# Kernel optimization log

Hardware: AMD Instinct MI355X
Metric: run time of the kernel (lower is better)

Reference implementation:

```python
import jax, jax.numpy as jnp
import numpy as np
import math

# Static config derived from init_kwargs
B, L, D, H, NL = 256, 256, 128, 2, 2
E = D // H                       # 64
F = L // 2 + 1                   # 129 rfft bins
SR = 0.6                         # sample_ratio (> 1/n_layers)
STEP = (F * (1.0 - SR)) // (NL - 1)          # 51.0, python float floor-div as in torch code
LEFTS = [int(F * (1.0 - SR) - k * STEP) for k in range(NL)]   # [51, 0]
RIGHTS = [int(F - k * STEP) for k in range(NL)]               # [129, 78]
TOPK = max(int(1 * math.log(L)), 1)          # factor=1 -> 5
NUM_TOTAL = 100000                           # user_num + item_num
SPATIAL_RATIO = 0.1
INV_SQRT_E = 1.0 / math.sqrt(E)
INV_SQRT_2 = 1.0 / math.sqrt(2.0)


def setup_inputs() -> dict:
    key = jax.random.key(0)
    ks = jax.random.split(key, 12)
    s = 0.05
    return {
        "paths": jax.random.randint(ks[0], (B, L), 0, NUM_TOTAL),
        "lengths": jax.random.randint(ks[1], (B,), 1, L + 1),
        "degrees": jax.random.randint(ks[2], (B,), 0, 64),
        "training": 1,
        "ego_emb": jax.random.normal(ks[3], (NUM_TOTAL + 1, D), jnp.float32) * s,
        "pos_emb": jax.random.normal(ks[4], (L, D), jnp.float32) * s,
        "Wq": jax.random.normal(ks[5], (NL, D, D), jnp.float32) * s,
        "Wk": jax.random.normal(ks[6], (NL, D, D), jnp.float32) * s,
        "Wv": jax.random.normal(ks[7], (NL, D, D), jnp.float32) * s,
        "Wp": jax.random.normal(ks[8], (NL, D, D), jnp.float32) * s,
        "F1": jax.random.normal(ks[9], (NL, D, 2 * D), jnp.float32) * s,
        "F2": jax.random.normal(ks[10], (NL, 2 * D, D), jnp.float32) * s,
    }


def _hybrid_attention(k, x, mask, Wq, Wk, Wv, Wp):
    # project and split heads: [B,H,E,L]
    def proj(W):
        return (x @ W).reshape(B, L, H, E).transpose(0, 2, 3, 1)
    q, kk, v = proj(Wq), proj(Wk), proj(Wv)
    qf = jnp.fft.rfft(q, axis=-1)   # [B,H,E,F] complex
    kf = jnp.fft.rfft(kk, axis=-1)
    vf = jnp.fft.rfft(v, axis=-1)
    l, r = LEFTS[k], RIGHTS[k]
    # frequency-band attention: band-limited cross-correlation (scatter back == zero-pad)
    res = qf[..., l:r] * jnp.conj(kf[..., l:r])
    box = jnp.zeros(qf.shape, dtype=res.dtype).at[..., l:r].set(res)
    corr = jnp.fft.irfft(box, n=L, axis=-1)          # [B,H,E,L]
    mean_value = jnp.mean(corr, axis=(1, 2))         # [B,L]
    # training branch: global topk delays (shared across batch), roll-based aggregation
    _, delays = jax.lax.top_k(jnp.mean(mean_value, axis=0), TOPK)   # [TOPK]
    weights = mean_value[:, delays]                  # [B,TOPK]
    tmp_corr = jax.nn.softmax(weights, axis=-1)      # [B,TOPK]
    # roll(v, -d) along time == gather at (t + d) % L
    idx = (jnp.arange(L)[None, :] + delays[:, None]) % L            # [TOPK,L]
    gathered = v[:, :, :, idx]                       # [B,H,E,TOPK,L]
    freq = jnp.einsum('bhetl,bt->bhel', gathered, tmp_corr)
    freq = freq.transpose(0, 3, 1, 2).reshape(B, L, D)
    # dual-domain: time attention on band-limited signals (std=True -> same band)
    def band_ifft(f):
        padded = jnp.zeros(f.shape, dtype=f.dtype).at[..., l:r].set(f[..., l:r])
        return jnp.fft.irfft(padded, n=L, axis=-1).transpose(0, 1, 3, 2)   # [B,H,L,E]
    qt, kt, vt = band_ifft(qf), band_ifft(kf), band_ifft(vf)
    scores = jnp.einsum('bhqe,bhke->bhqk', qt, kt) * INV_SQRT_E + mask
    att = jax.nn.softmax(scores, axis=-1)
    spatial = jnp.einsum('bhqk,bhke->bhqe', att, vt).transpose(0, 2, 1, 3).reshape(B, L, D)
    out = (1.0 - SPATIAL_RATIO) * freq + SPATIAL_RATIO * spatial
    return out @ Wp + x


def reference(paths, lengths, degrees, training, ego_emb, pos_emb, Wq, Wk, Wv, Wp, F1, F2):
    del degrees, training  # degrees unused; training branch baked in (training=True)
    x = ego_emb[paths] + pos_emb[None, :, :]         # [B,L,D]
    m = (paths < NUM_TOTAL).astype(jnp.float32)
    mask = ((1.0 - m) * -10000.0)[:, None, None, :]  # [B,1,1,L]
    for k in range(NL):
        a = _hybrid_attention(k, x, mask, Wq[k], Wk[k], Wv[k], Wp[k])
        h = a @ F1[k]
        h = h * 0.5 * (1.0 + jax.lax.erf(h * INV_SQRT_2))   # exact GELU
        x = h @ F2[k]
    # gather last valid position per sequence
    return x[jnp.arange(B), lengths - 1]             # [B,D]
```

## Files before the change

### kernel.cpp

```cpp
#include <hip/hip_runtime.h>
#include <math.h>

#define Bn 256
#define Ln 256
#define Dn 128
#define Hn 2
#define En 64
#define NLn 2
#define TOPKn 5
#define NUM_TOTALn 100000
#define BLD (Bn*Ln*Dn)
#define WT_LAYER 147456

using frag_ab = __attribute__((ext_vector_type(8))) short;
using frag_cd = __attribute__((ext_vector_type(4))) float;

__device__ inline short f2bf(float f) {
    union { float f; unsigned u; } c; c.f = f;
    unsigned r = (c.u + 0x7FFFu + ((c.u >> 16) & 1u)) >> 16;
    return (short)r;
}
__device__ inline float bf2f(short s) {
    union { unsigned u; float f; } c; c.u = ((unsigned)(unsigned short)s) << 16;
    return c.f;
}

__global__ void beacon_kernel(float* out, float v) { out[0] = v; }

__global__ __launch_bounds__(256) void build_G_kernel(short* __restrict__ G) {
    int k = blockIdx.x, t = blockIdx.y, s = threadIdx.x;
    int d = (t - s) & 255;
    int f1 = (k == 0) ? 51 : 1;
    int f2 = (k == 0) ? 127 : 77;
    float acc;
    if (d == 0) {
        acc = 2.0f * (float)(f2 - f1 + 1);
    } else {
        const float c = 3.14159265358979323846f / 256.0f;
        int ahi = (d * (2 * f2 + 1)) & 511;
        int alo = (d * (2 * f1 - 1)) & 511;
        acc = (sinf(c * (float)ahi) - sinf(c * (float)alo)) / sinf(c * (float)d);
    }
    acc += (k == 0) ? ((d & 1) ? -1.0f : 1.0f)
                    : 1.0f;
    G[((size_t)k * 256 + t) * 256 + s] = f2bf(acc * (1.0f / 256.0f));
}

__global__ __launch_bounds__(256) void build_x_kernel(const int* __restrict__ paths,
                                                      const float* __restrict__ ego,
                                                      const float* __restrict__ pos,
                                                      short* __restrict__ x) {
    int base = (blockIdx.x * 256 + threadIdx.x) * 4;
    int d = base & 127;
    int bl = base >> 7;
    int t = bl & 255;
    float4 e = *(const float4*)(ego + (size_t)paths[bl] * Dn + d);
    float4 p = *(const float4*)(pos + t * Dn + d);
    short4 s;
    s.x = f2bf(e.x + p.x); s.y = f2bf(e.y + p.y);
    s.z = f2bf(e.z + p.z); s.w = f2bf(e.w + p.w);
    *(short4*)&x[base] = s;
}

__global__ __launch_bounds__(256) void wtrans_all_kernel(
        const float* __restrict__ Wq, const float* __restrict__ Wk,
        const float* __restrict__ Wv, const float* __restrict__ Wp,
        const float* __restrict__ F1, const float* __restrict__ F2,
        short* __restrict__ Wt) {
    int z = blockIdx.y;
    int idx = blockIdx.x * 256 + threadIdx.x;
    short* WtL = Wt + (size_t)z * WT_LAYER;
    if (idx < 65536) {
        int which = idx >> 14, local = idx & 16383;
        const float* src = (which == 0) ? Wq : (which == 1) ? Wk
                         : (which == 2) ? Wv : Wp;
        float scale = (which == 3) ? 0.1f : 1.0f;
        int n = local & 127, k = local >> 7;
        WtL[(which << 14) + n * 128 + k] = f2bf(scale * src[(size_t)z * 16384 + local]);
    } else if (idx < 98304) {
        int local = idx - 65536;
        int n = local & 255, k = local >> 8;
        WtL[65536 + n * 128 + k] = f2bf(F1[(size_t)z * 32768 + local]);
    } else {
        int local = idx - 98304;
        int n = local & 127, k = local >> 7;
        WtL[98304 + n * 256 + k] = f2bf(F2[(size_t)z * 32768 + local]);
    }
}

template<bool BT_FAST, bool GELU_EPI>
__global__ __launch_bounds__(256)
void mfma_gemm_kernel(const short* A, const short* Bp, short* C, const short* R,
                      int K, int lda, int ldb, int ldc, int ldr,
                      long long sA, long long sB, long long sC, long long sR,
                      long long sCsplit, float alpha, float beta) {
    int bz = blockIdx.z;
    A += (size_t)bz * sA; C += (size_t)bz * sC;
    if (R) R += (size_t)bz * sR;
    const short* Bt = Bp + (size_t)bz * sB;
    const int m0 = blockIdx.x * 128, n0 = blockIdx.y * 128;
    int n0c = n0;
    if (sCsplit) { C += (size_t)blockIdx.y * sCsplit; n0c = 0; }
    __shared__ short As[128 * 40];
    __shared__ short Bs[128 * 40];
    int tid = threadIdx.x;
    int lane = tid & 63, wave = tid >> 6;
    int wr = (wave >> 1) * 64, wc = (wave & 1) * 64;
    int l15 = lane & 15, qd = lane >> 4;

    frag_cd zero4 = {0.f, 0.f, 0.f, 0.f};
    frag_cd acc[4][4];
    #pragma unroll
    for (int i = 0; i < 4; i++)
        #pragma unroll
        for (int j = 0; j < 4; j++) acc[i][j] = zero4;

    int arow = tid >> 1, acg = (tid & 1) * 16;
    int bnrow = tid >> 1, bcg = (tid & 1) * 16;
    int bkk = tid & 31, bnb = (tid >> 5) * 16;

    int4 pa0, pa1, pb0, pb1;
    {
        const short* ap = A + (size_t)(m0 + arow) * lda + acg;
        pa0 = *(const int4*)ap; pa1 = *(const int4*)(ap + 8);
        if (BT_FAST) {
            const short* bp = Bt + (size_t)(n0 + bnrow) * ldb + bcg;
            pb0 = *(const int4*)bp; pb1 = *(const int4*)(bp + 8);
        } else {
            const short* bp = Bt + (size_t)bkk * ldb + n0 + bnb;
            pb0 = *(const int4*)bp; pb1 = *(const int4*)(bp + 8);
        }
    }

    for (int k0 = 0; k0 < K; k0 += 32) {
        __syncthreads();
        *(int4*)&As[arow * 40 + acg] = pa0;
        *(int4*)&As[arow * 40 + acg + 8] = pa1;
        if (BT_FAST) {
            *(int4*)&Bs[bnrow * 40 + bcg] = pb0;
            *(int4*)&Bs[bnrow * 40 + bcg + 8] = pb1;
        } else {
            short tmp[16];
            *(int4*)&tmp[0] = pb0; *(int4*)&tmp[8] = pb1;
            #pragma unroll
            for (int i = 0; i < 16; i++) Bs[(bnb + i) * 40 + bkk] = tmp[i];
        }
        __syncthreads();
        if (k0 + 32 < K) {
            const short* ap = A + (size_t)(m0 + arow) * lda + k0 + 32 + acg;
            pa0 = *(const int4*)ap; pa1 = *(const int4*)(ap + 8);
            if (BT_FAST) {
                const short* bp = Bt + (size_t)(n0 + bnrow) * ldb + k0 + 32 + bcg;
                pb0 = *(const int4*)bp; pb1 = *(const int4*)(bp + 8);
            } else {
                const short* bp = Bt + (size_t)(k0 + 32 + bkk) * ldb + n0 + bnb;
                pb0 = *(const int4*)bp; pb1 = *(const int4*)(bp + 8);
            }
        }
        frag_ab af[4], bf[4];
        #pragma unroll
        for (int ms = 0; ms < 4; ms++)
            af[ms] = *(frag_ab*)&As[(wr + ms * 16 + l15) * 40 + qd * 8];
        #pragma unroll
        for (int ns = 0; ns < 4; ns++)
            bf[ns] = *(frag_ab*)&Bs[(wc + ns * 16 + l15) * 40 + qd * 8];
        #pragma unroll
        for (int ms = 0; ms < 4; ms++)
            #pragma unroll
            for (int ns = 0; ns < 4; ns++)
                acc[ms][ns] = __builtin_amdgcn_mfma_f32_16x16x32_bf16(
                    bf[ns], af[ms], acc[ms][ns], 0, 0, 0);
    }
    #pragma unroll
    for (int ms = 0; ms < 4; ms++) {
        int m = m0 + wr + ms * 16 + l15;
        #pragma unroll
        for (int ns = 0; ns < 4; ns++) {
            int nb = wc + ns * 16 + qd * 4;
            float v[4];
            #pragma unroll
            for (int r = 0; r < 4; r++) v[r] = alpha * acc[ms][ns][r];
            if (R) {
                short4 r4 = *(const short4*)&R[(size_t)m * ldr + n0 + nb];
                v[0] += beta * bf2f(r4.x); v[1] += beta * bf2f(r4.y);
                v[2] += beta * bf2f(r4.z); v[3] += beta * bf2f(r4.w);
            }
            if (GELU_EPI) {
                #pragma unroll
                for (int r = 0; r < 4; r++)
                    v[r] = v[r] * 0.5f * (1.0f + erff(v[r] * 0.70710678118654752f));
            }
            short4 o;
            o.x = f2bf(v[0]); o.y = f2bf(v[1]); o.z = f2bf(v[2]); o.w = f2bf(v[3]);
            *(short4*)&C[(size_t)m * ldc + n0c + nb] = o;
        }
    }
}

static inline void mgemm(hipStream_t s, const short* A, const short* B, short* C,
                         const short* R, int M, int N, int K,
                         int lda, int ldb, int ldc, int ldr,
                         long long sA, long long sB, long long sC, long long sR,
                         int batch, float alpha, float beta, bool btFast, bool gelu,
                         long long sCsplit = 0) {
    dim3 grid(M / 128, N / 128, batch), block(256);
    if (btFast) {
        if (gelu) mfma_gemm_kernel<true, true ><<<grid, block, 0, s>>>(A, B, C, R, K, lda, ldb, ldc, ldr, sA, sB, sC, sR, sCsplit, alpha, beta);
        else      mfma_gemm_kernel<true, false><<<grid, block, 0, s>>>(A, B, C, R, K, lda, ldb, ldc, ldr, sA, sB, sC, sR, sCsplit, alpha, beta);
    } else {
        if (gelu) mfma_gemm_kernel<false, true ><<<grid, block, 0, s>>>(A, B, C, R, K, lda, ldb, ldc, ldr, sA, sB, sC, sR, sCsplit, alpha, beta);
        else      mfma_gemm_kernel<false, false><<<grid, block, 0, s>>>(A, B, C, R, K, lda, ldb, ldc, ldr, sA, sB, sC, sR, sCsplit, alpha, beta);
    }
}

__global__ __launch_bounds__(512)
void filtproj_kernel(const short* __restrict__ G, const short* __restrict__ x,
                     const short* __restrict__ W, short* __restrict__ q) {
    int b = blockIdx.x;
    __shared__ short As[256 * 40];
    __shared__ short Bs[128 * 40];
    __shared__ short xf[256 * 136];
    int tid = threadIdx.x;
    int lane = tid & 63, wave = tid >> 6;
    int wr = (wave & 3) * 64, wc = (wave >> 2) * 64;
    int l15 = lane & 15, qd = lane >> 4;
    const short* xb = x + ((size_t)b << 15);

    frag_cd zero4 = {0.f, 0.f, 0.f, 0.f};
    frag_cd acc[4][4];
    #pragma unroll
    for (int i = 0; i < 4; i++)
        #pragma unroll
        for (int j = 0; j < 4; j++) acc[i][j] = zero4;

    int arow = tid >> 1, acg = (tid & 1) * 16;
    int bkk = tid & 31, bnb = (tid >> 5) * 16;

    int4 pa0, pa1, pb0, pb1;
    {
        const short* ap = G + (size_t)arow * 256 + acg;
        pa0 = *(const int4*)ap; pa1 = *(const int4*)(ap + 8);
        if (tid < 256) {
            const short* bp = xb + (size_t)bkk * 128 + bnb;
            pb0 = *(const int4*)bp; pb1 = *(const int4*)(bp + 8);
        }
    }
    for (int k0 = 0; k0 < 256; k0 += 32) {
        __syncthreads();
        *(int4*)&As[arow * 40 + acg] = pa0;
        *(int4*)&As[arow * 40 + acg + 8] = pa1;
        if (tid < 256) {
            short tmp[16];
            *(int4*)&tmp[0] = pb0; *(int4*)&tmp[8] = pb1;
            #pragma unroll
            for (int i = 0; i < 16; i++) Bs[(bnb + i) * 40 + bkk] = tmp[i];
        }
        __syncthreads();
        if (k0 + 32 < 256) {
            const short* ap = G + (size_t)arow * 256 + k0 + 32 + acg;
            pa0 = *(const int4*)ap; pa1 = *(const int4*)(ap + 8);
            if (tid < 256) {
                const short* bp = xb + (size_t)(k0 + 32 + bkk) * 128 + bnb;
                pb0 = *(const int4*)bp; pb1 = *(const int4*)(bp + 8);
            }
        }
        frag_ab af[4], bf[4];
        #pragma unroll
        for (int ms = 0; ms < 4; ms++)
            af[ms] = *(frag_ab*)&As[(wr + ms * 16 + l15) * 40 + qd * 8];
        #pragma unroll
        for (int ns = 0; ns < 4; ns++)
            bf[ns] = *(frag_ab*)&Bs[(wc + ns * 16 + l15) * 40 + qd * 8];
        #pragma unroll
        for (int ms = 0; ms < 4; ms++)
            #pragma unroll
            for (int ns = 0; ns < 4; ns++)
                acc[ms][ns] = __builtin_amdgcn_mfma_f32_16x16x32_bf16(
                    bf[ns], af[ms], acc[ms][ns], 0, 0, 0);
    }
    #pragma unroll
    for (int ms = 0; ms < 4; ms++) {
        int m = wr + ms * 16 + l15;
        #pragma unroll
        for (int ns = 0; ns < 4; ns++) {
            int nb = wc + ns * 16 + qd * 4;
            short4 o;
            o.x = f2bf(acc[ms][ns][0]); o.y = f2bf(acc[ms][ns][1]);
            o.z = f2bf(acc[ms][ns][2]); o.w = f2bf(acc[ms][ns][3]);
            *(short4*)&xf[m * 136 + nb] = o;
        }
    }

    int brow = tid >> 2, bcg = (tid & 3) * 8;
    #pragma unroll 1
    for (int y = 0; y < 3; y++) {
        const short* Bt = W + y * 16384;
        #pragma unroll
        for (int i = 0; i < 4; i++)
            #pragma unroll
            for (int j = 0; j < 4; j++) acc[i][j] = zero4;
        int4 pb = *(const int4*)(Bt + (size_t)brow * 128 + bcg);
        for (int k0 = 0; k0 < 128; k0 += 32) {
            __syncthreads();
            *(int4*)&Bs[brow * 40 + bcg] = pb;
            __syncthreads();
            if (k0 + 32 < 128)
                pb = *(const int4*)(Bt + (size_t)brow * 128 + k0 + 32 + bcg);
            frag_ab af[4], bf[4];
            #pragma unroll
            for (int ms = 0; ms < 4; ms++)
                af[ms] = *(frag_ab*)&xf[(wr + ms * 16 + l15) * 136 + k0 + qd * 8];
            #pragma unroll
            for (int ns = 0; ns < 4; ns++)
                bf[ns] = *(frag_ab*)&Bs[(wc + ns * 16 + l15) * 40 + qd * 8];
            #pragma unroll
            for (int ms = 0; ms < 4; ms++)
                #pragma unroll
                for (int ns = 0; ns < 4; ns++)
                    acc[ms][ns] = __builtin_amdgcn_mfma_f32_16x16x32_bf16(
                        bf[ns], af[ms], acc[ms][ns], 0, 0, 0);
        }
        short* Cy = q + (size_t)y * BLD + ((size_t)b << 15);
        #pragma unroll
        for (int ms = 0; ms < 4; ms++) {
            int m = wr + ms * 16 + l15;
            #pragma unroll
            for (int ns = 0; ns < 4; ns++) {
                int nb = wc + ns * 16 + qd * 4;
                short4 o;
                o.x = f2bf(acc[ms][ns][0]); o.y = f2bf(acc[ms][ns][1]);
                o.z = f2bf(acc[ms][ns][2]); o.w = f2bf(acc[ms][ns][3]);
                *(short4*)&Cy[(size_t)m * 128 + nb] = o;
            }
        }
    }
}

template<bool DUAL, bool GELU_EPI, bool MIXA>
__global__ __launch_bounds__(512)
void bgemm_kernel(const short* __restrict__ A1, const short* __restrict__ B1, int K1,
                  const short* __restrict__ A2, const short* __restrict__ B2, int K2,
                  short* C, const short* __restrict__ R, int ldc, int ldr,
                  long long sCsplit,
                  const float* __restrict__ tc, const int* __restrict__ delays) {
    const int m0 = blockIdx.x * 256;
    int n0c;
    if (sCsplit) { C += (size_t)blockIdx.y * sCsplit; n0c = 0; }
    else         { n0c = blockIdx.y * 128; }
    __shared__ short As[256 * 40];
    __shared__ short Bs[128 * 40];
    int tid = threadIdx.x;
    int lane = tid & 63, wave = tid >> 6;
    int wr = (wave & 3) * 64, wc = (wave >> 2) * 64;
    int l15 = lane & 15, qd = lane >> 4;

    float wj[TOPKn]; int dj[TOPKn];
    if (MIXA) {
        #pragma unroll
        for (int j = 0; j < TOPKn; j++) {
            wj[j] = tc[blockIdx.x * TOPKn + j];
            dj[j] = delays[j];
        }
    }

    frag_cd zero4 = {0.f, 0.f, 0.f, 0.f};
    frag_cd acc[4][4];
    #pragma unroll
    for (int i = 0; i < 4; i++)
        #pragma unroll
        for (int j = 0; j < 4; j++) acc[i][j] = zero4;

    int arow = tid >> 1, acg = (tid & 1) * 16;
    int brow = tid >> 2, bcg = (tid & 3) * 8;

    #pragma unroll
    for (int pass = 0; pass < (DUAL ? 2 : 1); pass++) {
        const short* A = pass ? A2 : A1;
        const short* Bb = (pass ? B2 : B1);
        int K = pass ? K2 : K1;
        const bool domix = MIXA && (pass == 0);
        const short* Bt = Bb + (size_t)blockIdx.y * 128 * K;
        const short* xb = A + ((size_t)m0 << 7);
        int4 pa0, pa1, pb0;
        {
            if (!domix) {
                const short* ap = A + (size_t)(m0 + arow) * K + acg;
                pa0 = *(const int4*)ap; pa1 = *(const int4*)(ap + 8);
            }
            pb0 = *(const int4*)(Bt + (size_t)brow * K + bcg);
        }
        for (int k0 = 0; k0 < K; k0 += 32) {
            __syncthreads();
            if (domix) {
                #pragma unroll
                for (int c = 0; c < 2; c++) {
                    int col = k0 + acg + c * 8;
                    float m8[8] = {0.f, 0.f, 0.f, 0.f, 0.f, 0.f, 0.f, 0.f};
                    #pragma unroll
                    for (int j = 0; j < TOPKn; j++) {
                        frag_ab v = *(const frag_ab*)(xb + (((arow + dj[j]) & 255) << 7) + col);
                        #pragma unroll
                        for (int i = 0; i < 8; i++) m8[i] += wj[j] * bf2f(v[i]);
                    }
                    frag_ab o;
                    #pragma unroll
                    for (int i = 0; i < 8; i++) o[i] = f2bf(m8[i]);
                    *(frag_ab*)&As[arow * 40 + acg + c * 8] = o;
                }
            } else {
                *(int4*)&As[arow * 40 + acg] = pa0;
                *(int4*)&As[arow * 40 + acg + 8] = pa1;
            }
            *(int4*)&Bs[brow * 40 + bcg] = pb0;
            __syncthreads();
            if (k0 + 32 < K) {
                if (!domix) {
                    const short* ap = A + (size_t)(m0 + arow) * K + k0 + 32 + acg;
                    pa0 = *(const int4*)ap; pa1 = *(const int4*)(ap + 8);
                }
                pb0 = *(const int4*)(Bt + (size_t)brow * K + k0 + 32 + bcg);
            }
            frag_ab af[4], bf[4];
            #pragma unroll
            for (int ms = 0; ms < 4; ms++)
                af[ms] = *(frag_ab*)&As[(wr + ms * 16 + l15) * 40 + qd * 8];
            #pragma unroll
            for (int ns = 0; ns < 4; ns++)
                bf[ns] = *(frag_ab*)&Bs[(wc + ns * 16 + l15) * 40 + qd * 8];
            #pragma unroll
            for (int ms = 0; ms < 4; ms++)
                #pragma unroll
                for (int ns = 0; ns < 4; ns++)
                    acc[ms][ns] = __builtin_amdgcn_mfma_f32_16x16x32_bf16(
                        bf[ns], af[ms], acc[ms][ns], 0, 0, 0);
        }
    }
    #pragma unroll
    for (int ms = 0; ms < 4; ms++) {
        int m = m0 + wr + ms * 16 + l15;
        #pragma unroll
        for (int ns = 0; ns < 4; ns++) {
            int nb = wc + ns * 16 + qd * 4;
            float v[4];
            #pragma unroll
            for (int r = 0; r < 4; r++) v[r] = acc[ms][ns][r];
            if (R) {
                short4 r4 = *(const short4*)&R[(size_t)m * ldr + n0c + nb];
                v[0] += bf2f(r4.x); v[1] += bf2f(r4.y);
                v[2] += bf2f(r4.z); v[3] += bf2f(r4.w);
            }
            if (GELU_EPI) {
                #pragma unroll
                for (int r = 0; r < 4; r++)
                    v[r] = v[r] * 0.5f * (1.0f + erff(v[r] * 0.70710678118654752f));
            }
            short4 o;
            o.x = f2bf(v[0]); o.y = f2bf(v[1]); o.z = f2bf(v[2]); o.w = f2bf(v[3]);
            *(short4*)&C[(size_t)m * ldc + n0c + nb] = o;
        }
    }
}

__global__ __launch_bounds__(512, 4) void attn_kernel(short* q,
        const short* __restrict__ kb, const short* __restrict__ vf,
        const int* __restrict__ paths, float* __restrict__ mv2) {
    int h = blockIdx.x, b = blockIdx.y;
    __shared__ short SB[256 * 72];
    __shared__ short ks[64 * 72];
    __shared__ short vT[80 * 72];
    __shared__ float masks[256];
    __shared__ float mvpart[512];
    int tid = threadIdx.x;
    int lane = tid & 63, wave = tid >> 6;
    int l15 = lane & 15, qd = lane >> 4;
    if (tid < 256) masks[tid] = (paths[b * 256 + tid] < NUM_TOTALn) ? 0.0f : -10000.0f;
    {
        int e0 = tid * 2;
        #pragma unroll
        for (int i = 0; i < 2; i++) {
            int e = e0 + i;
            int row = 64 + (e >> 6), col = e & 63;
            vT[row * 72 + col] = (row == 64) ? (short)0x3F80 : (short)0;
        }
    }
    short* qg = q + ((size_t)b << 15) + (size_t)h * 64;
    const short* kg = kb + ((size_t)b << 15) + (size_t)h * 64;
    const short* vg = vf + ((size_t)b << 15) + (size_t)h * 64;

    #pragma unroll
    for (int p = 0; p < 4; p++) {
        int chunk = p * 512 + tid;
        int r = chunk >> 3, cb = (chunk & 7) * 8;
        *(frag_ab*)&SB[r * 72 + cb] = *(const frag_ab*)(qg + (size_t)r * 128 + cb);
    }
    __syncthreads();
    int myrow = wave * 32;
    frag_ab aq[2][2];
    #pragma unroll
    for (int mt = 0; mt < 2; mt++)
        #pragma unroll
        for (int hf = 0; hf < 2; hf++)
            aq[mt][hf] = *(frag_ab*)&SB[(myrow + mt * 16 + l15) * 72 + hf * 32 + qd * 8];

    frag_cd zero4 = {0.f, 0.f, 0.f, 0.f};
    frag_cd oacc[2][5];
    #pragma unroll
    for (int mt = 0; mt < 2; mt++)
        #pragma unroll
        for (int et = 0; et < 5; et++) oacc[mt][et] = zero4;
    float macc = 0.0f;
    int tau = tid & 255, half = tid >> 8;

    for (int jt = 0; jt < 4; jt++) {
        __syncthreads();
        {
            int r = tid >> 3, cb = (tid & 7) * 8;
            *(frag_ab*)&ks[r * 72 + cb] =
                *(const frag_ab*)(kg + (size_t)(jt * 64 + r) * 128 + cb);
            frag_ab v8 = *(const frag_ab*)(vg + (size_t)(jt * 64 + r) * 128 + cb);
            int swz = (((r >> 3) ^ (cb >> 3)) << 3) + (r & 7);
            #pragma unroll
            for (int i = 0; i < 8; i++) vT[(cb + i) * 72 + swz] = v8[i];
        }
        __syncthreads();
        #pragma unroll
        for (int mt = 0; mt < 2; mt++) {
            #pragma unroll
            for (int nt = 0; nt < 4; nt++) {
                frag_ab b0 = *(frag_ab*)&ks[(nt * 16 + l15) * 72 + qd * 8];
                frag_ab b1 = *(frag_ab*)&ks[(nt * 16 + l15) * 72 + 32 + qd * 8];
                frag_cd c = zero4;
                c = __builtin_amdgcn_mfma_f32_16x16x32_bf16(aq[mt][0], b0, c, 0, 0, 0);
                c = __builtin_amdgcn_mfma_f32_16x16x32_bf16(aq[mt][1], b1, c, 0, 0, 0);
                int keyLocal = nt * 16 + l15;
                #pragma unroll
                for (int r = 0; r < 4; r++) {
                    int row = myrow + mt * 16 + qd * 4 + r;
                    int tt = (row - jt * 64 - keyLocal) & 255;
                    SB[tt * 66 + keyLocal] = f2bf(c[r] * 0.125f);
                }
            }
        }
        __syncthreads();
        {
            const int* SD32 = (const int*)&SB[tau * 66 + half * 32];
            #pragma unroll
            for (int i = 0; i < 16; i++) {
                int pk = SD32[i];
                macc += bf2f((short)(pk & 0xFFFF)) + bf2f((short)(pk >> 16));
            }
        }
        #pragma unroll
        for (int mt = 0; mt < 2; mt++) {
            int row = myrow + mt * 16 + l15;
            #pragma unroll
            for (int hf = 0; hf < 2; hf++) {
                int kl0 = hf * 32 + qd * 8;
                frag_ab pfrag;
                #pragma unroll
                for (int j = 0; j < 8; j++) {
                    int kl = kl0 + j;
                    int tt = (row - jt * 64 - kl) & 255;
                    float s = bf2f(SB[tt * 66 + kl]);
                    pfrag[j] = f2bf(__expf(s + masks[jt * 64 + kl]));
                }
                #pragma unroll
                for (int et = 0; et < 5; et++) {
                    int e = et * 16 + l15;
                    int blk = (hf * 4 + qd) ^ ((e >> 3) & 7);
                    frag_ab bv = *(frag_ab*)&vT[e * 72 + (blk << 3)];
                    oacc[mt][et] = __builtin_amdgcn_mfma_f32_16x16x32_bf16(pfrag, bv, oacc[mt][et], 0, 0, 0);
                }
            }
        }
    }
    __syncthreads();
    mvpart[tid] = macc;
    __syncthreads();
    if (tid < 256)
        mv2[(size_t)h * 65536 + b * 256 + tid] =
            (mvpart[tid] + mvpart[tid + 256]) * 0.0625f;
    #pragma unroll
    for (int mt = 0; mt < 2; mt++) {
        #pragma unroll
        for (int r = 0; r < 4; r++) {
            float l = oacc[mt][4][r];
            l = __shfl(l, (lane & 48));
            float inv = 1.0f / l;
            int row = myrow + mt * 16 + qd * 4 + r;
            #pragma unroll
            for (int et = 0; et < 4; et++)
                qg[(size_t)row * 128 + et * 16 + l15] = f2bf(oacc[mt][et][r] * inv);
        }
    }
}

__global__ __launch_bounds__(256) void gm_reduce_kernel(const float* __restrict__ mv2,
                                                        float* __restrict__ gm) {
    int tau = blockIdx.x;
    int b = threadIdx.x;
    __shared__ float red[256];
    red[b] = mv2[b * 256 + tau] + mv2[65536 + b * 256 + tau];
    __syncthreads();
    for (int s = 128; s > 0; s >>= 1) { if (b < s) red[b] += red[b + s]; __syncthreads(); }
    if (b == 0) gm[tau] = red[0] * (1.0f / 256.0f);
}

__global__ __launch_bounds__(256) void topk_softmax_kernel(const float* __restrict__ gm,
                                                           const float* __restrict__ mv2,
                                                           int* __restrict__ delays,
                                                           float* __restrict__ tc) {
    __shared__ float vsh[4];
    __shared__ int ish[4];
    __shared__ int dsh[TOPKn];
    int tid = threadIdx.x;
    int lane = tid & 63, wave = tid >> 6;
    float v = gm[tid];
    for (int t = 0; t < TOPKn; t++) {
        float mv_ = v; int mi = tid;
        #pragma unroll
        for (int s = 32; s > 0; s >>= 1) {
            float v2 = __shfl_xor(mv_, s); int i2 = __shfl_xor(mi, s);
            if (v2 > mv_ || (v2 == mv_ && i2 < mi)) { mv_ = v2; mi = i2; }
        }
        if (lane == 0) { vsh[wave] = mv_; ish[wave] = mi; }
        __syncthreads();
        if (tid == 0) {
            float bv = vsh[0]; int bi = ish[0];
            #pragma unroll
            for (int w = 1; w < 4; w++)
                if (vsh[w] > bv || (vsh[w] == bv && ish[w] < bi)) { bv = vsh[w]; bi = ish[w]; }
            dsh[t] = bi; delays[t] = bi;
        }
        __syncthreads();
        if (tid == dsh[t]) v = -1e30f;
    }
    __syncthreads();
    int b = tid;
    float w[TOPKn];
    float m = -1e30f;
    #pragma unroll
    for (int j = 0; j < TOPKn; j++) {
        w[j] = mv2[b * 256 + dsh[j]] + mv2[65536 + b * 256 + dsh[j]];
        m = fmaxf(m, w[j]);
    }
    float ssum = 0.0f;
    #pragma unroll
    for (int j = 0; j < TOPKn; j++) { w[j] = expf(w[j] - m); ssum += w[j]; }
    #pragma unroll
    for (int j = 0; j < TOPKn; j++) tc[b * TOPKn + j] = w[j] / ssum;
}

__global__ __launch_bounds__(256) void gather_out_kernel(const short* __restrict__ x,
                                                         const int* __restrict__ lengths,
                                                         float* __restrict__ out) {
    int idx = blockIdx.x * 256 + threadIdx.x;
    int d = idx & 127;
    int b = idx >> 7;
    out[idx] = bf2f(x[((size_t)b << 15) + (size_t)(lengths[b] - 1) * Dn + d]);
}

extern "C" void kernel_launch(void* const* d_in, const int* in_sizes, int n_in,
                              void* d_out, int out_size, void* d_ws, size_t ws_size,
                              hipStream_t stream) {
    const int* paths    = (const int*)d_in[0];
    const int* lengths  = (const int*)d_in[1];
    const float* ego    = (const float*)d_in[4];
    const float* pos    = (const float*)d_in[5];
    const float* Wq     = (const float*)d_in[6];
    const float* Wk     = (const float*)d_in[7];
    const float* Wv     = (const float*)d_in[8];
    const float* Wp     = (const float*)d_in[9];
    const float* F1     = (const float*)d_in[10];
    const float* F2     = (const float*)d_in[11];
    float* out = (float*)d_out;

    const size_t need = (size_t)5 * BLD * 2 + 131072 * 2 + 131072 * 4
                        + 256 * 4 + 1280 * 4 + 16 * 4 + (size_t)NLn * WT_LAYER * 2;
    if (ws_size < need) {
        beacon_kernel<<<dim3(1), dim3(1), 0, stream>>>(out, (float)(ws_size >> 20));
        return;
    }

    short* x    = (short*)d_ws;
    short* q    = x + (size_t)1 * BLD;
    short* kb   = x + (size_t)2 * BLD;
    short* vf   = x + (size_t)3 * BLD;
    short* x5   = x + (size_t)4 * BLD;
    short* Gb   = x + (size_t)5 * BLD;
    float* mv   = (float*)(Gb + 131072);
    float* gm   = mv + 131072;
    float* tc   = gm + 256;
    int* delays = (int*)(tc + 1280);
    short* Wt   = (short*)(delays + 16);

    build_G_kernel<<<dim3(2, 256), dim3(256), 0, stream>>>(Gb);
    build_x_kernel<<<dim3(BLD / 1024), dim3(256), 0, stream>>>(paths, ego, pos, x);

    wtrans_all_kernel<<<dim3(512, NLn), dim3(256), 0, stream>>>(Wq, Wk, Wv, Wp, F1, F2, Wt);
    mgemm(stream, Wt + 49152, Wt + 32768, Wt + 131072, nullptr,
          128, 128, 128, 128, 128, 128, 0,
          WT_LAYER, WT_LAYER, WT_LAYER, 0, NLn,
          9.0f, 0.0f, false, false);

    for (int k = 0; k < NLn; k++) {
        const short* WtL = Wt + (size_t)k * WT_LAYER;
        filtproj_kernel<<<dim3(256), dim3(512), 0, stream>>>(
            Gb + (size_t)k * 65536, x, WtL, q);

        attn_kernel<<<dim3(2, 256), dim3(512), 0, stream>>>(q, kb, vf, paths, mv);

        gm_reduce_kernel<<<dim3(256), dim3(256), 0, stream>>>(mv, gm);
        topk_softmax_kernel<<<dim3(1), dim3(256), 0, stream>>>(gm, mv, delays, tc);

        bgemm_kernel<true, false, true><<<dim3(256, 1), dim3(512), 0, stream>>>(
            x, WtL + 131072, 128, q, WtL + 49152, 128, kb, x, 128, 128, 0,
            tc, delays);
        bgemm_kernel<false, true, false><<<dim3(256, 2), dim3(512), 0, stream>>>(
            kb, WtL + 65536, 128, nullptr, nullptr, 0, vf, nullptr, 256, 0, 0,
            nullptr, nullptr);
        bgemm_kernel<false, false, false><<<dim3(256, 1), dim3(512), 0, stream>>>(
            vf, WtL + 98304, 256, nullptr, nullptr, 0, x, nullptr, 128, 0, 0,
            nullptr, nullptr);
    }

    gather_out_kernel<<<dim3((Bn * Dn) / 256), dim3(256), 0, stream>>>(x, lengths, out);
}
```

Baseline: 378.4 us.

## Fuse FFN up-projection, GELU and down-projection into one kernel

Replaces the two FFN GEMM launches (F1 with GELU epilogue, then F2) with a single kernel per 256-row tile. The GELU-activated hidden activations stay in shared memory in two 128-column halves, which avoids writing and rereading the 256-wide intermediate through global memory and saves one launch per layer. In exchange the block uses about 140KB of shared memory, which limits occupancy to one block per CU, and the FFN now runs on 256 blocks instead of 512+256.

```diff
diff --git a/kernel.cpp b/kernel.cpp
--- a/kernel.cpp
+++ b/kernel.cpp
@@ -336,6 +336,124 @@
     }
 }
 
+__global__ __launch_bounds__(512)
+void ffn_kernel(const short* __restrict__ a, const short* __restrict__ W,
+                short* __restrict__ x) {
+    int b = blockIdx.x;
+    __shared__ short aL[256 * 132];
+    __shared__ short hA[256 * 132];
+    __shared__ short Bs[128 * 36];
+    int tid = threadIdx.x;
+    int lane = tid & 63, wave = tid >> 6;
+    int wr = (wave & 3) * 64, wc = (wave >> 2) * 64;
+    int l15 = lane & 15, qd = lane >> 4;
+    const short* ab = a + ((size_t)b << 15);
+    const short* F1T = W + 65536;
+    const short* F2T = W + 98304;
+
+    #pragma unroll
+    for (int p = 0; p < 8; p++) {
+        int chunk = p * 512 + tid;
+        int r = chunk >> 4, cb = (chunk & 15) * 8;
+        *(frag_ab*)&aL[r * 132 + cb] = *(const frag_ab*)(ab + (size_t)r * 128 + cb);
+    }
+
+    frag_cd zero4 = {0.f, 0.f, 0.f, 0.f};
+    frag_cd xacc[4][4];
+    #pragma unroll
+    for (int i = 0; i < 4; i++)
+        #pragma unroll
+        for (int j = 0; j < 4; j++) xacc[i][j] = zero4;
+
+    int brow = tid >> 2, bcg = (tid & 3) * 8;
+
+    #pragma unroll 1
+    for (int half = 0; half < 2; half++) {
+        const short* B1 = F1T + (size_t)(half * 128) * 128;
+        frag_cd acc[4][4];
+        #pragma unroll
+        for (int i = 0; i < 4; i++)
+            #pragma unroll
+            for (int j = 0; j < 4; j++) acc[i][j] = zero4;
+        int4 pb = *(const int4*)(B1 + (size_t)brow * 128 + bcg);
+        for (int k0 = 0; k0 < 128; k0 += 32) {
+            __syncthreads();
+            *(int4*)&Bs[brow * 36 + bcg] = pb;
+            __syncthreads();
+            if (k0 + 32 < 128)
+                pb = *(const int4*)(B1 + (size_t)brow * 128 + k0 + 32 + bcg);
+            frag_ab af[4], bf[4];
+            #pragma unroll
+            for (int ms = 0; ms < 4; ms++)
+                af[ms] = *(frag_ab*)&aL[(wr + ms * 16 + l15) * 132 + k0 + qd * 8];
+            #pragma unroll
+            for (int ns = 0; ns < 4; ns++)
+                bf[ns] = *(frag_ab*)&Bs[(wc + ns * 16 + l15) * 36 + qd * 8];
+            #pragma unroll
+            for (int ms = 0; ms < 4; ms++)
+                #pragma unroll
+                for (int ns = 0; ns < 4; ns++)
+                    acc[ms][ns] = __builtin_amdgcn_mfma_f32_16x16x32_bf16(
+                        bf[ns], af[ms], acc[ms][ns], 0, 0, 0);
+        }
+        __syncthreads();
+        #pragma unroll
+        for (int ms = 0; ms < 4; ms++) {
+            int m = wr + ms * 16 + l15;
+            #pragma unroll
+            for (int ns = 0; ns < 4; ns++) {
+                int nb = wc + ns * 16 + qd * 4;
+                float v[4];
+                #pragma unroll
+                for (int r = 0; r < 4; r++) {
+                    float t = acc[ms][ns][r];
+                    v[r] = t * 0.5f * (1.0f + erff(t * 0.70710678118654752f));
+                }
+                short4 o;
+                o.x = f2bf(v[0]); o.y = f2bf(v[1]);
+                o.z = f2bf(v[2]); o.w = f2bf(v[3]);
+                *(short4*)&hA[m * 132 + nb] = o;
+            }
+        }
+        __syncthreads();
+
+        int4 pb2 = *(const int4*)(F2T + (size_t)brow * 256 + half * 128 + bcg);
+        for (int k0 = 0; k0 < 128; k0 += 32) {
+            __syncthreads();
+            *(int4*)&Bs[brow * 36 + bcg] = pb2;
+            __syncthreads();
+            if (k0 + 32 < 128)
+                pb2 = *(const int4*)(F2T + (size_t)brow * 256 + half * 128 + k0 + 32 + bcg);
+            frag_ab af[4], bf[4];
+            #pragma unroll
+            for (int ms = 0; ms < 4; ms++)
+                af[ms] = *(frag_ab*)&hA[(wr + ms * 16 + l15) * 132 + k0 + qd * 8];
+            #pragma unroll
+            for (int ns = 0; ns < 4; ns++)
+                bf[ns] = *(frag_ab*)&Bs[(wc + ns * 16 + l15) * 36 + qd * 8];
+            #pragma unroll
+            for (int ms = 0; ms < 4; ms++)
+                #pragma unroll
+                for (int ns = 0; ns < 4; ns++)
+                    xacc[ms][ns] = __builtin_amdgcn_mfma_f32_16x16x32_bf16(
+                        bf[ns], af[ms], xacc[ms][ns], 0, 0, 0);
+        }
+    }
+    short* xb = x + ((size_t)b << 15);
+    #pragma unroll
+    for (int ms = 0; ms < 4; ms++) {
+        int m = wr + ms * 16 + l15;
+        #pragma unroll
+        for (int ns = 0; ns < 4; ns++) {
+            int nb = wc + ns * 16 + qd * 4;
+            short4 o;
+            o.x = f2bf(xacc[ms][ns][0]); o.y = f2bf(xacc[ms][ns][1]);
+            o.z = f2bf(xacc[ms][ns][2]); o.w = f2bf(xacc[ms][ns][3]);
+            *(short4*)&xb[(size_t)m * 128 + nb] = o;
+        }
+    }
+}
+
 template<bool DUAL, bool GELU_EPI, bool MIXA>
 __global__ __launch_bounds__(512)
 void bgemm_kernel(const short* __restrict__ A1, const short* __restrict__ B1, int K1,
@@ -686,7 +804,6 @@
     short* q    = x + (size_t)1 * BLD;
     short* kb   = x + (size_t)2 * BLD;
     short* vf   = x + (size_t)3 * BLD;
-    short* x5   = x + (size_t)4 * BLD;
     short* Gb   = x + (size_t)5 * BLD;
     float* mv   = (float*)(Gb + 131072);
     float* gm   = mv + 131072;
@@ -716,12 +833,7 @@
         bgemm_kernel<true, false, true><<<dim3(256, 1), dim3(512), 0, stream>>>(
             x, WtL + 131072, 128, q, WtL + 49152, 128, kb, x, 128, 128, 0,
             tc, delays);
-        bgemm_kernel<false, true, false><<<dim3(256, 2), dim3(512), 0, stream>>>(
-            kb, WtL + 65536, 128, nullptr, nullptr, 0, vf, nullptr, 256, 0, 0,
-            nullptr, nullptr);
-        bgemm_kernel<false, false, false><<<dim3(256, 1), dim3(512), 0, stream>>>(
-            vf, WtL + 98304, 256, nullptr, nullptr, 0, x, nullptr, 128, 0, 0,
-            nullptr, nullptr);
+        ffn_kernel<<<dim3(256), dim3(512), 0, stream>>>(kb, WtL, x);
     }
 
     gather_out_kernel<<<dim3((Bn * Dn) / 256), dim3(256), 0, stream>>>(x, lengths, out);
```

After: 360.3 us. 4.8% less time.
